# Kernel tuning notes

Hardware: AMD Instinct MI355X
Metric: run time of the kernel (lower is better)

## Reference

```python
import jax, jax.numpy as jnp
import numpy as np

H = 512  # hidden_dim


def setup_inputs() -> dict:
    key = jax.random.key(0)
    k1, k2, k3 = jax.random.split(key, 3)
    context = jax.random.normal(k1, (32, 512, H), dtype=jnp.float32)
    query = jax.random.normal(k2, (32, 64, H), dtype=jnp.float32)
    # similarity_linear.weight has shape (1, 3H); store flattened as (3H,)
    W = jax.random.normal(k3, (3 * H,), dtype=jnp.float32) * (1.0 / np.sqrt(3 * H))
    return {"context": context, "query": query, "W": W}


def reference(context, query, W):
    # Decompose W into the three blocks applied to [c, q, c*q].
    w_c, w_q, w_m = W[:H], W[H:2 * H], W[2 * H:]
    # S[b,i,j] = c_i.w_c + q_j.w_q + sum_d c_id * q_jd * w_m_d  -- same math as
    # Linear(3H,1) over cat([c_exp, q_exp, c_exp*q_exp]), without the O(B*C*Q*3H) tensor.
    s_c = context @ w_c                       # [B, C]
    s_q = query @ w_q                         # [B, Q]
    s_m = jnp.einsum('bcd,bqd->bcq', context * w_m, query)  # [B, C, Q]
    S = s_m + s_c[:, :, None] + s_q[:, None, :]              # [B, C, Q]

    a = jax.nn.softmax(S, axis=2)             # context-to-query attention
    attended_query = jnp.einsum('bcq,bqd->bcd', a, query)    # [B, C, H]

    b = jax.nn.softmax(jnp.max(S, axis=2), axis=1)           # [B, C]
    attended_context = jnp.einsum('bc,bcd->bd', b, context)  # [B, H]
    attended_context = jnp.broadcast_to(attended_context[:, None, :], context.shape)

    G = jnp.concatenate([
        context,
        attended_query,
        context * attended_query,
        context * attended_context,
    ], axis=2)  # [B, C, 4H]
    return G
```

## Files before the change

### kernel.cpp

```cpp
#include <hip/hip_runtime.h>
#include <cstdint>

#define NB 32
#define NC 512
#define NQ 64
#define ND 512

typedef __attribute__((ext_vector_type(8))) short bf16x8;
typedef __attribute__((ext_vector_type(4))) float f32x4;

__device__ __forceinline__ short f2bf(float f) {
  union { float f; unsigned u; } v; v.f = f;
  v.u += 0x7fffu + ((v.u >> 16) & 1u);
  return (short)(v.u >> 16);
}

__global__ __launch_bounds__(512) void kPrep(
    const float* __restrict__ qry, const float* __restrict__ W,
    short* __restrict__ qbf, short* __restrict__ qTbf, float* __restrict__ s_q)
{
  __shared__ short lq[NQ*ND];
  const int b = blockIdx.x;
  const int t = threadIdx.x;
  const int r = t >> 3;
  const int cb = (t & 7) * 64;
  const float* qrow = qry + ((size_t)(b*NQ + r))*ND + cb;
  float sq = 0.f;
  #pragma unroll
  for (int i = 0; i < 16; ++i) {
    const float4 qv = *(const float4*)(qrow + i*4);
    const float4 wv = *(const float4*)(W + ND + cb + i*4);
    sq += qv.x*wv.x + qv.y*wv.y + qv.z*wv.z + qv.w*wv.w;
    short4 s; s.x=f2bf(qv.x); s.y=f2bf(qv.y); s.z=f2bf(qv.z); s.w=f2bf(qv.w);
    *(short4*)&qbf[((size_t)(b*NQ + r))*ND + cb + i*4] = s;
    *(short4*)&lq[r*ND + cb + i*4] = s;
  }
  sq += __shfl_xor(sq, 1, 8); sq += __shfl_xor(sq, 2, 8); sq += __shfl_xor(sq, 4, 8);
  if ((t & 7) == 0) s_q[b*NQ + r] = sq;
  __syncthreads();
  const int d = t;
  short* qTrow = qTbf + ((size_t)(b*ND + d))*NQ;
  #pragma unroll
  for (int j = 0; j < 16; ++j) {
    short4 h;
    h.x = lq[(j*4+0)*ND + d];
    h.y = lq[(j*4+1)*ND + d];
    h.z = lq[(j*4+2)*ND + d];
    h.w = lq[(j*4+3)*ND + d];
    *(short4*)&qTrow[j*4] = h;
  }
}

__global__ __launch_bounds__(64) void kS(
    const float* __restrict__ ctx, const float* __restrict__ W,
    const short* __restrict__ qbf, const short* __restrict__ qTbf,
    const float* __restrict__ s_q, float* __restrict__ G, float* __restrict__ m_ws)
{
  __shared__ __align__(16) short P[16*72];
  __shared__ __align__(16) float aqf[16*68];
  __shared__ float scf[16];

  const int t    = threadIdx.x;
  const int ln15 = t & 15;
  const int g    = t >> 4;
  const int bid  = (int)blockIdx.x;
  const int swz  = (bid & 7) * 128 + (bid >> 3);
  const int b    = swz >> 5;
  const int c0   = (swz & 31) * 16;

  const float* crow = ctx + ((size_t)(b*NC + c0 + ln15))*ND;

  f32x4 acc[4] = {};
  float scp = 0.f;

  #pragma unroll 2
  for (int kc = 0; kc < 8; ++kc) {
    #pragma unroll
    for (int kk = 0; kk < 2; ++kk) {
      const int dd = kc*64 + kk*32 + g*8;
      const float4 c0v = *(const float4*)(crow + dd);
      const float4 c1v = *(const float4*)(crow + dd + 4);
      const float4 wc0 = *(const float4*)(W + dd);
      const float4 wc1 = *(const float4*)(W + dd + 4);
      const float4 wm0 = *(const float4*)(W + 2*ND + dd);
      const float4 wm1 = *(const float4*)(W + 2*ND + dd + 4);
      scp += c0v.x*wc0.x + c0v.y*wc0.y + c0v.z*wc0.z + c0v.w*wc0.w
           + c1v.x*wc1.x + c1v.y*wc1.y + c1v.z*wc1.z + c1v.w*wc1.w;
      bf16x8 a;
      a[0]=f2bf(c0v.x*wm0.x); a[1]=f2bf(c0v.y*wm0.y); a[2]=f2bf(c0v.z*wm0.z); a[3]=f2bf(c0v.w*wm0.w);
      a[4]=f2bf(c1v.x*wm1.x); a[5]=f2bf(c1v.y*wm1.y); a[6]=f2bf(c1v.z*wm1.z); a[7]=f2bf(c1v.w*wm1.w);
      #pragma unroll
      for (int n = 0; n < 4; ++n) {
        const bf16x8 bq = *(const bf16x8*)&qbf[((size_t)(b*NQ + n*16 + ln15))*ND + dd];
        acc[n] = __builtin_amdgcn_mfma_f32_16x16x32_bf16(a, bq, acc[n], 0, 0, 0);
      }
    }
  }

  scp += __shfl_xor(scp, 16, 64);
  scp += __shfl_xor(scp, 32, 64);
  if (g == 0) scf[ln15] = scp;
  __syncthreads();

  float sqv[4];
  #pragma unroll
  for (int n = 0; n < 4; ++n) sqv[n] = s_q[b*NQ + n*16 + ln15];

  #pragma unroll
  for (int reg = 0; reg < 4; ++reg) {
    const int rloc = g*4 + reg;
    float sv[4];
    #pragma unroll
    for (int n = 0; n < 4; ++n) sv[n] = acc[n][reg] + sqv[n];
    float mx = fmaxf(fmaxf(sv[0], sv[1]), fmaxf(sv[2], sv[3]));
    mx = fmaxf(mx, __shfl_xor(mx, 1, 16));
    mx = fmaxf(mx, __shfl_xor(mx, 2, 16));
    mx = fmaxf(mx, __shfl_xor(mx, 4, 16));
    mx = fmaxf(mx, __shfl_xor(mx, 8, 16));
    float s = 0.f;
    #pragma unroll
    for (int n = 0; n < 4; ++n) { sv[n] = __expf(sv[n] - mx); s += sv[n]; }
    s += __shfl_xor(s, 1, 16); s += __shfl_xor(s, 2, 16);
    s += __shfl_xor(s, 4, 16); s += __shfl_xor(s, 8, 16);
    const float inv = 1.0f / s;
    if (ln15 == 0) m_ws[b*NC + c0 + rloc] = mx + scf[rloc];
    #pragma unroll
    for (int n = 0; n < 4; ++n)
      P[rloc*72 + ln15 + 16*n] = f2bf(sv[n] * inv);
  }
  __syncthreads();

  bf16x8 pa[2];
  pa[0] = *(const bf16x8*)&P[ln15*72 + g*8];
  pa[1] = *(const bf16x8*)&P[ln15*72 + 32 + g*8];

  for (int dc = 0; dc < 8; ++dc) {
    const int d0 = dc * 64;
    f32x4 acc2[4] = {};
    #pragma unroll
    for (int kk = 0; kk < 2; ++kk)
      #pragma unroll
      for (int n = 0; n < 4; ++n) {
        const bf16x8 bq = *(const bf16x8*)&qTbf[((size_t)(b*ND + d0 + n*16 + ln15))*NQ + kk*32 + g*8];
        acc2[n] = __builtin_amdgcn_mfma_f32_16x16x32_bf16(pa[kk], bq, acc2[n], 0, 0, 0);
      }
    __syncthreads();
    #pragma unroll
    for (int n = 0; n < 4; ++n)
      #pragma unroll
      for (int reg = 0; reg < 4; ++reg)
        aqf[(g*4 + reg)*68 + n*16 + ln15] = acc2[n][reg];
    __syncthreads();
    #pragma unroll
    for (int pass = 0; pass < 4; ++pass) {
      const int r = pass*4 + g;
      const float4 aq4 = *(const float4*)&aqf[r*68 + ln15*4];
      const float4 cv  = *(const float4*)(ctx + ((size_t)(b*NC + c0 + r))*ND + d0 + ln15*4);
      float* gp = G + ((size_t)(b*NC + c0 + r))*2048 + d0 + ln15*4;
      *(float4*)(gp)        = cv;
      *(float4*)(gp + 512)  = aq4;
      *(float4*)(gp + 1024) = make_float4(cv.x*aq4.x, cv.y*aq4.y,
                                          cv.z*aq4.z, cv.w*aq4.w);
    }
  }
}

__global__ __launch_bounds__(256) void k2_partial(
    const float* __restrict__ ctx, const float* __restrict__ m_ws, float* __restrict__ pc)
{
  const int t  = threadIdx.x;
  const int b  = blockIdx.x >> 4;
  const int ch = blockIdx.x & 15;
  __shared__ float r8[8];
  __shared__ float wts[32];

  const float v0 = m_ws[b*NC + t];
  const float v1 = m_ws[b*NC + 256 + t];
  float mx = fmaxf(v0, v1);
  #pragma unroll
  for (int o = 32; o; o >>= 1) mx = fmaxf(mx, __shfl_xor(mx, o, 64));
  if ((t & 63) == 0) r8[t >> 6] = mx;
  __syncthreads();
  mx = fmaxf(fmaxf(r8[0], r8[1]), fmaxf(r8[2], r8[3]));
  float e = __expf(v0 - mx) + __expf(v1 - mx);
  #pragma unroll
  for (int o = 32; o; o >>= 1) e += __shfl_xor(e, o, 64);
  if ((t & 63) == 0) r8[4 + (t >> 6)] = e;
  __syncthreads();
  const float denom = r8[4] + r8[5] + r8[6] + r8[7];
  if (t < 32) wts[t] = __expf(m_ws[b*NC + ch*32 + t] - mx) / denom;
  __syncthreads();

  float s0 = 0.f, s1 = 0.f;
  const float* base = ctx + ((size_t)(b*NC + ch*32))*ND;
  for (int c = 0; c < 32; ++c) {
    const float w = wts[c];
    s0 += w * base[(size_t)c*ND + t];
    s1 += w * base[(size_t)c*ND + t + 256];
  }
  pc[((size_t)(b*16 + ch))*ND + t]       = s0;
  pc[((size_t)(b*16 + ch))*ND + t + 256] = s1;
}

__global__ __launch_bounds__(512) void k2_reduce(
    const float* __restrict__ pc, float* __restrict__ ac)
{
  const int b = blockIdx.x;
  const int d = threadIdx.x;
  float s = 0.f;
  #pragma unroll
  for (int ch = 0; ch < 16; ++ch) s += pc[((size_t)(b*16 + ch))*ND + d];
  ac[b*ND + d] = s;
}

__global__ __launch_bounds__(256) void kFinal(
    const float* __restrict__ ctx, const float* __restrict__ ac, float* __restrict__ G)
{
  const size_t e = ((size_t)blockIdx.x*256 + threadIdx.x) * 8;
  const int b = (int)(e >> 18);
  const int r = (int)(e & 262143);
  const int c = r >> 9;
  const int d = r & 511;
  const float4 x0 = *(const float4*)(ctx + e);
  const float4 x1 = *(const float4*)(ctx + e + 4);
  const float4 a0 = *(const float4*)(ac + b*ND + d);
  const float4 a1 = *(const float4*)(ac + b*ND + d + 4);
  float* gp = G + ((size_t)(b*NC + c))*2048 + 1536 + d;
  *(float4*)(gp)     = make_float4(x0.x*a0.x, x0.y*a0.y, x0.z*a0.z, x0.w*a0.w);
  *(float4*)(gp + 4) = make_float4(x1.x*a1.x, x1.y*a1.y, x1.z*a1.z, x1.w*a1.w);
}

extern "C" void kernel_launch(void* const* d_in, const int* in_sizes, int n_in,
                              void* d_out, int out_size, void* d_ws, size_t ws_size,
                              hipStream_t stream)
{
  const float* ctx = (const float*)d_in[0];
  const float* qry = (const float*)d_in[1];
  const float* W   = (const float*)d_in[2];
  float* G = (float*)d_out;

  float* ws   = (float*)d_ws;
  float* m_ws = ws;
  float* pc   = ws + 16384;
  float* ac   = ws + 278528;
  float* s_q  = ws + 294912;
  short* qbf  = (short*)(ws + 296960);
  short* qTbf = qbf + (size_t)NB*NQ*ND;

  kPrep     <<<dim3(NB),    dim3(512), 0, stream>>>(qry, W, qbf, qTbf, s_q);
  kS        <<<dim3(NB*32), dim3(64),  0, stream>>>(ctx, W, qbf, qTbf, s_q, G, m_ws);
  k2_partial<<<dim3(NB*16), dim3(256), 0, stream>>>(ctx, m_ws, pc);
  k2_reduce <<<dim3(NB),    dim3(512), 0, stream>>>(pc, ac);
  kFinal    <<<dim3((NB*NC*ND)/(256*8)), dim3(256), 0, stream>>>(ctx, ac, G);
}
```

Before: 77.02 us.

## Split kS across two waves and move context copy into final kernel

The S/attention kernel now runs with two wavefronts per block. Each wave computes half of the query columns, and a cross-wave softmax merge of partial max and sum goes through shared memory. Each wave also handles half of the hidden dimension in the attended-query stage. Writing the raw context slice of G moves from kS into kFinal, which already reads ctx, so kS no longer loads and stores that slice. The intent is to double per-CU parallelism on the MFMA-heavy kernel and cut redundant traffic, at the cost of an extra barrier and some duplicated context loads per wave.

```diff
diff --git a/kernel.cpp b/kernel.cpp
--- a/kernel.cpp
+++ b/kernel.cpp
@@ -51,18 +51,21 @@
   }
 }
 
-__global__ __launch_bounds__(64) void kS(
+__global__ __launch_bounds__(128) void kS(
     const float* __restrict__ ctx, const float* __restrict__ W,
     const short* __restrict__ qbf, const short* __restrict__ qTbf,
     const float* __restrict__ s_q, float* __restrict__ G, float* __restrict__ m_ws)
 {
   __shared__ __align__(16) short P[16*72];
-  __shared__ __align__(16) float aqf[16*68];
+  __shared__ __align__(16) float aqf[2][16*68];
+  __shared__ float pmL[2][16], peL[2][16];
   __shared__ float scf[16];
 
   const int t    = threadIdx.x;
-  const int ln15 = t & 15;
-  const int g    = t >> 4;
+  const int lane = t & 63;
+  const int w    = t >> 6;
+  const int ln15 = lane & 15;
+  const int g    = lane >> 4;
   const int bid  = (int)blockIdx.x;
   const int swz  = (bid & 7) * 128 + (bid >> 3);
   const int b    = swz >> 5;
@@ -70,7 +73,7 @@
 
   const float* crow = ctx + ((size_t)(b*NC + c0 + ln15))*ND;
 
-  f32x4 acc[4] = {};
+  f32x4 acc[2] = {};
   float scp = 0.f;
 
   #pragma unroll 2
@@ -80,53 +83,65 @@
       const int dd = kc*64 + kk*32 + g*8;
       const float4 c0v = *(const float4*)(crow + dd);
       const float4 c1v = *(const float4*)(crow + dd + 4);
-      const float4 wc0 = *(const float4*)(W + dd);
-      const float4 wc1 = *(const float4*)(W + dd + 4);
       const float4 wm0 = *(const float4*)(W + 2*ND + dd);
       const float4 wm1 = *(const float4*)(W + 2*ND + dd + 4);
-      scp += c0v.x*wc0.x + c0v.y*wc0.y + c0v.z*wc0.z + c0v.w*wc0.w
-           + c1v.x*wc1.x + c1v.y*wc1.y + c1v.z*wc1.z + c1v.w*wc1.w;
+      if (w == 0) {
+        const float4 wc0 = *(const float4*)(W + dd);
+        const float4 wc1 = *(const float4*)(W + dd + 4);
+        scp += c0v.x*wc0.x + c0v.y*wc0.y + c0v.z*wc0.z + c0v.w*wc0.w
+             + c1v.x*wc1.x + c1v.y*wc1.y + c1v.z*wc1.z + c1v.w*wc1.w;
+      }
       bf16x8 a;
       a[0]=f2bf(c0v.x*wm0.x); a[1]=f2bf(c0v.y*wm0.y); a[2]=f2bf(c0v.z*wm0.z); a[3]=f2bf(c0v.w*wm0.w);
       a[4]=f2bf(c1v.x*wm1.x); a[5]=f2bf(c1v.y*wm1.y); a[6]=f2bf(c1v.z*wm1.z); a[7]=f2bf(c1v.w*wm1.w);
       #pragma unroll
-      for (int n = 0; n < 4; ++n) {
-        const bf16x8 bq = *(const bf16x8*)&qbf[((size_t)(b*NQ + n*16 + ln15))*ND + dd];
+      for (int n = 0; n < 2; ++n) {
+        const bf16x8 bq = *(const bf16x8*)&qbf[((size_t)(b*NQ + w*32 + n*16 + ln15))*ND + dd];
         acc[n] = __builtin_amdgcn_mfma_f32_16x16x32_bf16(a, bq, acc[n], 0, 0, 0);
       }
     }
   }
 
-  scp += __shfl_xor(scp, 16, 64);
-  scp += __shfl_xor(scp, 32, 64);
-  if (g == 0) scf[ln15] = scp;
-  __syncthreads();
-
-  float sqv[4];
-  #pragma unroll
-  for (int n = 0; n < 4; ++n) sqv[n] = s_q[b*NQ + n*16 + ln15];
+  if (w == 0) {
+    scp += __shfl_xor(scp, 16, 64);
+    scp += __shfl_xor(scp, 32, 64);
+    if (g == 0) scf[ln15] = scp;
+  }
+
+  float sqv[2];
+  #pragma unroll
+  for (int n = 0; n < 2; ++n) sqv[n] = s_q[b*NQ + w*32 + n*16 + ln15];
+
+  float ev0[4], ev1[4], pmr[4];
+  #pragma unroll
+  for (int reg = 0; reg < 4; ++reg) {
+    float sv0 = acc[0][reg] + sqv[0];
+    float sv1 = acc[1][reg] + sqv[1];
+    float pm = fmaxf(sv0, sv1);
+    pm = fmaxf(pm, __shfl_xor(pm, 1, 16));
+    pm = fmaxf(pm, __shfl_xor(pm, 2, 16));
+    pm = fmaxf(pm, __shfl_xor(pm, 4, 16));
+    pm = fmaxf(pm, __shfl_xor(pm, 8, 16));
+    const float e0 = __expf(sv0 - pm), e1 = __expf(sv1 - pm);
+    float pe = e0 + e1;
+    pe += __shfl_xor(pe, 1, 16); pe += __shfl_xor(pe, 2, 16);
+    pe += __shfl_xor(pe, 4, 16); pe += __shfl_xor(pe, 8, 16);
+    ev0[reg] = e0; ev1[reg] = e1; pmr[reg] = pm;
+    if (ln15 == 0) { pmL[w][g*4 + reg] = pm; peL[w][g*4 + reg] = pe; }
+  }
+  __syncthreads();
 
   #pragma unroll
   for (int reg = 0; reg < 4; ++reg) {
     const int rloc = g*4 + reg;
-    float sv[4];
-    #pragma unroll
-    for (int n = 0; n < 4; ++n) sv[n] = acc[n][reg] + sqv[n];
-    float mx = fmaxf(fmaxf(sv[0], sv[1]), fmaxf(sv[2], sv[3]));
-    mx = fmaxf(mx, __shfl_xor(mx, 1, 16));
-    mx = fmaxf(mx, __shfl_xor(mx, 2, 16));
-    mx = fmaxf(mx, __shfl_xor(mx, 4, 16));
-    mx = fmaxf(mx, __shfl_xor(mx, 8, 16));
-    float s = 0.f;
-    #pragma unroll
-    for (int n = 0; n < 4; ++n) { sv[n] = __expf(sv[n] - mx); s += sv[n]; }
-    s += __shfl_xor(s, 1, 16); s += __shfl_xor(s, 2, 16);
-    s += __shfl_xor(s, 4, 16); s += __shfl_xor(s, 8, 16);
-    const float inv = 1.0f / s;
-    if (ln15 == 0) m_ws[b*NC + c0 + rloc] = mx + scf[rloc];
-    #pragma unroll
-    for (int n = 0; n < 4; ++n)
-      P[rloc*72 + ln15 + 16*n] = f2bf(sv[n] * inv);
+    const float m0 = pmL[0][rloc], m1 = pmL[1][rloc];
+    const float s0 = peL[0][rloc], s1 = peL[1][rloc];
+    const float M  = fmaxf(m0, m1);
+    const float S  = s0*__expf(m0 - M) + s1*__expf(m1 - M);
+    const float f  = __expf(pmr[reg] - M) / S;
+    if (w == 0 && ln15 == 0) m_ws[b*NC + c0 + rloc] = M + scf[rloc];
+    P[rloc*72 + w*32 + ln15]      = f2bf(ev0[reg] * f);
+    P[rloc*72 + w*32 + 16 + ln15] = f2bf(ev1[reg] * f);
   }
   __syncthreads();
 
@@ -134,8 +149,8 @@
   pa[0] = *(const bf16x8*)&P[ln15*72 + g*8];
   pa[1] = *(const bf16x8*)&P[ln15*72 + 32 + g*8];
 
-  for (int dc = 0; dc < 8; ++dc) {
-    const int d0 = dc * 64;
+  for (int dc = 0; dc < 4; ++dc) {
+    const int d0 = w*256 + dc*64;
     f32x4 acc2[4] = {};
     #pragma unroll
     for (int kk = 0; kk < 2; ++kk)
@@ -149,15 +164,14 @@
     for (int n = 0; n < 4; ++n)
       #pragma unroll
       for (int reg = 0; reg < 4; ++reg)
-        aqf[(g*4 + reg)*68 + n*16 + ln15] = acc2[n][reg];
+        aqf[w][(g*4 + reg)*68 + n*16 + ln15] = acc2[n][reg];
     __syncthreads();
     #pragma unroll
     for (int pass = 0; pass < 4; ++pass) {
       const int r = pass*4 + g;
-      const float4 aq4 = *(const float4*)&aqf[r*68 + ln15*4];
+      const float4 aq4 = *(const float4*)&aqf[w][r*68 + ln15*4];
       const float4 cv  = *(const float4*)(ctx + ((size_t)(b*NC + c0 + r))*ND + d0 + ln15*4);
       float* gp = G + ((size_t)(b*NC + c0 + r))*2048 + d0 + ln15*4;
-      *(float4*)(gp)        = cv;
       *(float4*)(gp + 512)  = aq4;
       *(float4*)(gp + 1024) = make_float4(cv.x*aq4.x, cv.y*aq4.y,
                                           cv.z*aq4.z, cv.w*aq4.w);
@@ -225,9 +239,11 @@
   const float4 x1 = *(const float4*)(ctx + e + 4);
   const float4 a0 = *(const float4*)(ac + b*ND + d);
   const float4 a1 = *(const float4*)(ac + b*ND + d + 4);
-  float* gp = G + ((size_t)(b*NC + c))*2048 + 1536 + d;
-  *(float4*)(gp)     = make_float4(x0.x*a0.x, x0.y*a0.y, x0.z*a0.z, x0.w*a0.w);
-  *(float4*)(gp + 4) = make_float4(x1.x*a1.x, x1.y*a1.y, x1.z*a1.z, x1.w*a1.w);
+  float* gp = G + ((size_t)(b*NC + c))*2048 + d;
+  *(float4*)(gp)            = x0;
+  *(float4*)(gp + 4)        = x1;
+  *(float4*)(gp + 1536)     = make_float4(x0.x*a0.x, x0.y*a0.y, x0.z*a0.z, x0.w*a0.w);
+  *(float4*)(gp + 1536 + 4) = make_float4(x1.x*a1.x, x1.y*a1.y, x1.z*a1.z, x1.w*a1.w);
 }
 
 extern "C" void kernel_launch(void* const* d_in, const int* in_sizes, int n_in,
@@ -248,7 +264,7 @@
   short* qTbf = qbf + (size_t)NB*NQ*ND;
 
   kPrep     <<<dim3(NB),    dim3(512), 0, stream>>>(qry, W, qbf, qTbf, s_q);
-  kS        <<<dim3(NB*32), dim3(64),  0, stream>>>(ctx, W, qbf, qTbf, s_q, G, m_ws);
+  kS        <<<dim3(NB*32), dim3(128), 0, stream>>>(ctx, W, qbf, qTbf, s_q, G, m_ws);
   k2_partial<<<dim3(NB*16), dim3(256), 0, stream>>>(ctx, m_ws, pc);
   k2_reduce <<<dim3(NB),    dim3(512), 0, stream>>>(pc, ac);
   kFinal    <<<dim3((NB*NC*ND)/(256*8)), dim3(256), 0, stream>>>(ctx, ac, G);
```

Measured after the change: 82.17 us. +6.7%, slower.
